# Kernel tuning notes

Hardware: AMD Instinct MI355X
Metric: run time of the kernel (lower is better)

Reference implementation:

```python
import jax, jax.numpy as jnp
import numpy as np

B, IN, H = 4096, 2048, 2048
STD = 1.0 / np.sqrt(H)


def setup_inputs() -> dict:
    key = jax.random.key(0)
    ks = jax.random.split(key, 16)
    uni = lambda k, shape: jax.random.uniform(k, shape, jnp.float32, -STD, STD)
    inp = {
        "x": jax.random.normal(ks[0], (B, IN), jnp.float32),
        "h": jax.random.normal(ks[1], (B, H), jnp.float32),
        "c": jax.random.normal(ks[2], (B, H), jnp.float32),
        # weights are used untransposed via th.mm(x, w): w_x* must be [IN, H]-compatible,
        # which in the original requires IN == H; shapes kept as [H, IN].
        "w_xi": uni(ks[3], (H, IN)), "w_xf": uni(ks[4], (H, IN)),
        "w_xo": uni(ks[5], (H, IN)), "w_xc": uni(ks[6], (H, IN)),
        "w_hi": uni(ks[7], (H, H)), "w_hf": uni(ks[8], (H, H)),
        "w_ho": uni(ks[9], (H, H)), "w_hc": uni(ks[10], (H, H)),
        "b_i": uni(ks[11], (H,)), "b_f": uni(ks[12], (H,)),
        "b_o": uni(ks[13], (H,)), "b_c": uni(ks[14], (H,)),
    }
    return inp


def reference(x, h, c, w_xi, w_xf, w_xo, w_xc, w_hi, w_hf, w_ho, w_hc,
              b_i, b_f, b_o, b_c):
    # Fused form of the 8 small GEMMs: concat gate weights along output dim.
    Wx = jnp.concatenate([w_xi, w_xf, w_xo, w_xc], axis=1)  # [IN, 4H]
    Wh = jnp.concatenate([w_hi, w_hf, w_ho, w_hc], axis=1)  # [H, 4H]
    b = jnp.concatenate([b_i, b_f, b_o, b_c])               # [4H]
    gates = x @ Wx + h @ Wh + b                              # [B, 4H]
    i_t, f_t, o_t, g_t = jnp.split(gates, 4, axis=1)
    i_t = jax.nn.sigmoid(i_t)
    f_t = jax.nn.sigmoid(f_t)
    o_t = jax.nn.sigmoid(o_t)
    g_t = jnp.tanh(g_t)
    c_t = c * f_t + i_t * g_t
    h_t = o_t * jnp.tanh(c_t)
    # original reshapes to [B, 1, H]
    return h_t[:, None, :], c_t[:, None, :]
```

## Files before the change

kernel.cpp:

```cpp
#include <hip/hip_runtime.h>
#include <stdint.h>

typedef unsigned short u16;
typedef __bf16 bf16x8 __attribute__((ext_vector_type(8)));
typedef float f32x4 __attribute__((ext_vector_type(4)));
typedef unsigned short u16x8 __attribute__((ext_vector_type(8)));
typedef unsigned short u16x4 __attribute__((ext_vector_type(4)));

#define B_ROWS 4096
#define H_DIM  2048
#define K_DIM  4096
#define N_DIM  8192

__device__ __forceinline__ u16 f2b(float f) {
  union { float f; unsigned int i; } v; v.f = f;
  unsigned int i = v.i;
  return (u16)((i + 0x7fffu + ((i >> 16) & 1u)) >> 16);
}
__device__ __forceinline__ float b2f(u16 u) {
  union { unsigned int i; float f; } v; v.i = ((unsigned int)u) << 16; return v.f;
}
__device__ __forceinline__ float sigmoidf_(float x) { return 1.0f / (1.0f + __expf(-x)); }
__device__ __forceinline__ float tanhf_(float x)    { return 1.0f - 2.0f / (__expf(2.0f * x) + 1.0f); }

__device__ __forceinline__ void glds16(const u16* g, u16* l) {
  __builtin_amdgcn_global_load_lds(
      (__attribute__((address_space(1))) void*)(g),
      (__attribute__((address_space(3))) void*)(l), 16, 0, 0);
}

__device__ __forceinline__ uint32_t lds_off(const void* p) {
  return (uint32_t)(uintptr_t)(__attribute__((address_space(3))) const void*)p;
}

__device__ __forceinline__ bf16x8 ds_read128(uint32_t byte_off) {
  bf16x8 r;
  asm volatile("ds_read_b128 %0, %1" : "=&v"(r) : "v"(byte_off));
  return r;
}
__device__ __forceinline__ bf16x8 ds_read128_hi(uint32_t byte_off) {
  bf16x8 r;
  asm volatile("ds_read_b128 %0, %1 offset:4096" : "=&v"(r) : "v"(byte_off));
  return r;
}
#define SCHED_FENCE __builtin_amdgcn_sched_barrier(0)

struct WPtrs { const float* p[8]; };

__global__ __launch_bounds__(256) void prep_all(WPtrs wp,
                                                const float* __restrict__ X,
                                                const float* __restrict__ Hs,
                                                u16* __restrict__ Wt,
                                                u16* __restrict__ Abf) {
  __shared__ float tile[64][65];
  const int z = blockIdx.z;
  const int tid = threadIdx.x;
  if (z < 8) {
    const int s = z >> 2, g = z & 3;
    const float* __restrict__ w = wp.p[z];
    const int j0 = blockIdx.x * 64, k0 = blockIdx.y * 64;

    const int c4 = (tid & 15) * 4;
    const int r0 = tid >> 4;
#pragma unroll
    for (int it = 0; it < 4; ++it) {
      int r = r0 + it * 16;
      float4 v = *(const float4*)(w + (size_t)(k0 + r) * H_DIM + j0 + c4);
      tile[r][c4 + 0] = v.x;
      tile[r][c4 + 1] = v.y;
      tile[r][c4 + 2] = v.z;
      tile[r][c4 + 3] = v.w;
    }
    __syncthreads();

    const int cc = (tid & 7) * 8;
    const int jr0 = tid >> 3;
#pragma unroll
    for (int it = 0; it < 2; ++it) {
      int jr = jr0 + it * 32;
      u16x8 v;
#pragma unroll
      for (int i = 0; i < 8; ++i) v[i] = f2b(tile[cc + i][jr]);
      size_t orow = (size_t)(g * H_DIM + j0 + jr);
      *(u16x8*)(Wt + orow * K_DIM + (size_t)(s * H_DIM + k0 + cc)) = v;
    }
  } else {
    const int cid = (z - 8) * 1024 + blockIdx.y * 32 + blockIdx.x;
#pragma unroll
    for (int t = 0; t < 4; ++t) {
      const size_t chunk = (size_t)cid * 1024 + t * 256 + tid;
      const int b = (int)(chunk >> 9);
      const int c = ((int)chunk & 511) * 8;
      const float* src = (c < H_DIM) ? (X + (size_t)b * H_DIM + c)
                                     : (Hs + (size_t)b * H_DIM + (c - H_DIM));
      float4 v0 = *(const float4*)(src);
      float4 v1 = *(const float4*)(src + 4);
      u16x8 o;
      o[0] = f2b(v0.x); o[1] = f2b(v0.y); o[2] = f2b(v0.z); o[3] = f2b(v0.w);
      o[4] = f2b(v1.x); o[5] = f2b(v1.y); o[6] = f2b(v1.z); o[7] = f2b(v1.w);
      *(u16x8*)(Abf + chunk * 8) = o;
    }
  }
}

__global__ __launch_bounds__(512, 2) void gemm_gates(const u16* __restrict__ A,
                                                     const u16* __restrict__ Wt,
                                                     u16* __restrict__ gates) {
  __shared__ __align__(16) u16 sA[4 * 256 * 32];
  __shared__ __align__(16) u16 sB[4 * 256 * 32];
  const int tid = threadIdx.x;
  const int wave = tid >> 6, lane = tid & 63;
  const int wm = wave >> 2, wn = wave & 3;

  const int wg = (blockIdx.x & 7) * 64 + (blockIdx.x >> 3);
  const int bm = wg & 15;
  const int bn = wg >> 4;

  const int c0 = wave * 2;
  const int rs0 = c0 * 16 + (lane >> 2);
  const int rs1 = rs0 + 16;
  const int kc0 = (lane & 3) ^ ((rs0 >> 1) & 3);
  const int kc1 = (lane & 3) ^ ((rs1 >> 1) & 3);
  const size_t gA0 = (size_t)(bm * 256 + rs0) * K_DIM + kc0 * 8;
  const size_t gA1 = (size_t)(bm * 256 + rs1) * K_DIM + kc1 * 8;
  const size_t gB0 = (size_t)(bn * 256 + rs0) * K_DIM + kc0 * 8;
  const size_t gB1 = (size_t)(bn * 256 + rs1) * K_DIM + kc1 * 8;

  const int q = lane >> 4;
  uint32_t aOffB[4], bOffB[4];
#pragma unroll
  for (int i = 0; i < 4; ++i) {
    int ra = wm * 128 + i * 16 + (lane & 15);
    aOffB[i] = (uint32_t)(ra * 32 + ((q ^ ((ra >> 1) & 3)) * 8)) * 2u;
  }
#pragma unroll
  for (int i = 0; i < 4; ++i) {
    int rb = wn * 64 + i * 16 + (lane & 15);
    bOffB[i] = (uint32_t)(rb * 32 + ((q ^ ((rb >> 1) & 3)) * 8)) * 2u;
  }
  const uint32_t sAb = lds_off(sA);
  const uint32_t sBb = lds_off(sB);

  f32x4 acc[8][4] = {};
  const int NT = K_DIM / 32;

  bf16x8 af[4], ag[4], bfE[4], bfO[4];

#pragma unroll
  for (int t = 0; t < 3; ++t) {
    const size_t ko = (size_t)t * 32;
    u16* da = sA + t * 8192;
    u16* db = sB + t * 8192;
    glds16(A  + gA0 + ko, da + c0 * 512);
    glds16(A  + gA1 + ko, da + (c0 + 1) * 512);
    glds16(Wt + gB0 + ko, db + c0 * 512);
    glds16(Wt + gB1 + ko, db + (c0 + 1) * 512);
  }
  asm volatile("s_waitcnt vmcnt(8)" ::: "memory");
  __builtin_amdgcn_s_barrier();
  SCHED_FENCE;
#pragma unroll
  for (int i = 0; i < 4; ++i) af[i]  = ds_read128(sAb + aOffB[i]);
#pragma unroll
  for (int i = 0; i < 4; ++i) bfE[i] = ds_read128(sBb + bOffB[i]);

#define TILE_BODY(T, BFC, BFN)                                                 \
  {                                                                            \
    const int pf = (T) + 3;                                                    \
    const uint32_t aSlot = sAb + (uint32_t)((T) & 3) * 16384u;                 \
    const bool dopf = pf < NT;                                                 \
    const size_t ko = (size_t)pf * 32;                                         \
    if (dopf) {                                                                \
      u16* dA = sA + (pf & 3) * 8192;                                          \
      glds16(A + gA0 + ko, dA + c0 * 512);                                     \
      glds16(A + gA1 + ko, dA + (c0 + 1) * 512);                               \
    }                                                                          \
                                       \
    _Pragma("unroll")                                                          \
    for (int i = 0; i < 4; ++i) ag[i] = ds_read128_hi(aSlot + aOffB[i]);       \
     \
    asm volatile("s_waitcnt lgkmcnt(4)" ::: "memory");                         \
    SCHED_FENCE;                                                               \
    __builtin_amdgcn_s_setprio(1);                                             \
    _Pragma("unroll")                                                          \
    for (int mi = 0; mi < 4; ++mi)                                             \
      _Pragma("unroll")                                                        \
      for (int ni = 0; ni < 4; ++ni)                                           \
        acc[mi][ni] = __builtin_amdgcn_mfma_f32_16x16x32_bf16(                 \
            af[mi], BFC[ni], acc[mi][ni], 0, 0, 0);                            \
    __builtin_amdgcn_s_setprio(0);                                             \
    if (dopf) {                                                                \
      u16* dB = sB + (pf & 3) * 8192;                                          \
      glds16(Wt + gB0 + ko, dB + c0 * 512);                                    \
      glds16(Wt + gB1 + ko, dB + (c0 + 1) * 512);                              \
    }                                                                          \
       \
    if ((T) < NT - 3)       { asm volatile("s_waitcnt vmcnt(8) lgkmcnt(0)" ::: "memory"); } \
    else if ((T) == NT - 3) { asm volatile("s_waitcnt vmcnt(4) lgkmcnt(0)" ::: "memory"); } \
    else if ((T) == NT - 2) { asm volatile("s_waitcnt vmcnt(0) lgkmcnt(0)" ::: "memory"); } \
    else                    { asm volatile("s_waitcnt lgkmcnt(0)" ::: "memory"); }          \
    if ((T) < NT - 1) __builtin_amdgcn_s_barrier();                            \
    SCHED_FENCE;                                                               \
                                  \
    if ((T) + 1 < NT) {                                                        \
      const uint32_t aN = sAb + (uint32_t)(((T) + 1) & 3) * 16384u;            \
      const uint32_t bN = sBb + (uint32_t)(((T) + 1) & 3) * 16384u;            \
      _Pragma("unroll")                                                        \
      for (int i = 0; i < 4; ++i) af[i]  = ds_read128(aN + aOffB[i]);          \
      _Pragma("unroll")                                                        \
      for (int i = 0; i < 4; ++i) BFN[i] = ds_read128(bN + bOffB[i]);          \
    }                                                                          \
                   \
    __builtin_amdgcn_s_setprio(1);                                             \
    _Pragma("unroll")                                                          \
    for (int mi = 0; mi < 4; ++mi)                                             \
      _Pragma("unroll")                                                        \
      for (int ni = 0; ni < 4; ++ni)                                           \
        acc[4 + mi][ni] = __builtin_amdgcn_mfma_f32_16x16x32_bf16(             \
            ag[mi], BFC[ni], acc[4 + mi][ni], 0, 0, 0);                        \
    __builtin_amdgcn_s_setprio(0);                                             \
  }

  for (int T2 = 0; T2 < NT; T2 += 2) {
    TILE_BODY(T2,     bfE, bfO);
    TILE_BODY(T2 + 1, bfO, bfE);
  }
#undef TILE_BODY

  const int rbase = bm * 256 + wm * 128 + (lane >> 4) * 4;
  const int cbase = bn * 256 + wn * 64 + (lane & 15);
#pragma unroll
  for (int mi = 0; mi < 8; ++mi) {
#pragma unroll
    for (int ni = 0; ni < 4; ++ni) {
      size_t base = (size_t)(rbase + mi * 16) * N_DIM + (size_t)(cbase + ni * 16);
#pragma unroll
      for (int r = 0; r < 4; ++r)
        gates[base + (size_t)r * N_DIM] = f2b(acc[mi][ni][r]);
    }
  }
}

__global__ __launch_bounds__(256) void lstm_epilogue(
    const u16* __restrict__ gates, const float* __restrict__ Cin,
    const float* __restrict__ Bi, const float* __restrict__ Bf,
    const float* __restrict__ Bo, const float* __restrict__ Bc,
    float* __restrict__ Out) {
  const int idx = blockIdx.x * 256 + threadIdx.x;
  const int b = idx >> 9;
  const int j = (idx & 511) * 4;
  const size_t gbase = (size_t)b * N_DIM + j;
  u16x4 iv = *(const u16x4*)(gates + gbase);
  u16x4 fv = *(const u16x4*)(gates + gbase + 2048);
  u16x4 ov = *(const u16x4*)(gates + gbase + 4096);
  u16x4 gv = *(const u16x4*)(gates + gbase + 6144);
  float4 cv  = *(const float4*)(Cin + (size_t)b * H_DIM + j);
  float4 biv = *(const float4*)(Bi + j);
  float4 bfv = *(const float4*)(Bf + j);
  float4 bov = *(const float4*)(Bo + j);
  float4 bcv = *(const float4*)(Bc + j);
  float ce[4] = {cv.x, cv.y, cv.z, cv.w};
  float bie[4] = {biv.x, biv.y, biv.z, biv.w};
  float bfe[4] = {bfv.x, bfv.y, bfv.z, bfv.w};
  float boe[4] = {bov.x, bov.y, bov.z, bov.w};
  float bce[4] = {bcv.x, bcv.y, bcv.z, bcv.w};
  float4 hv, ctv;
  float he[4], cte[4];
#pragma unroll
  for (int e = 0; e < 4; ++e) {
    float it = sigmoidf_(b2f(iv[e]) + bie[e]);
    float ft = sigmoidf_(b2f(fv[e]) + bfe[e]);
    float ot = sigmoidf_(b2f(ov[e]) + boe[e]);
    float gt = tanhf_(b2f(gv[e]) + bce[e]);
    float ct = ce[e] * ft + it * gt;
    he[e] = ot * tanhf_(ct);
    cte[e] = ct;
  }
  hv.x = he[0]; hv.y = he[1]; hv.z = he[2]; hv.w = he[3];
  ctv.x = cte[0]; ctv.y = cte[1]; ctv.z = cte[2]; ctv.w = cte[3];
  *(float4*)(Out + (size_t)b * H_DIM + j) = hv;
  *(float4*)(Out + (size_t)B_ROWS * H_DIM + (size_t)b * H_DIM + j) = ctv;
}

extern "C" void kernel_launch(void* const* d_in, const int* in_sizes, int n_in,
                              void* d_out, int out_size, void* d_ws, size_t ws_size,
                              hipStream_t stream) {
  const float* X   = (const float*)d_in[0];
  const float* Hs  = (const float*)d_in[1];
  const float* Cin = (const float*)d_in[2];
  WPtrs wp;
  for (int i = 0; i < 8; ++i) wp.p[i] = (const float*)d_in[3 + i];
  const float* Bi = (const float*)d_in[11];
  const float* Bf = (const float*)d_in[12];
  const float* Bo = (const float*)d_in[13];
  const float* Bc = (const float*)d_in[14];

  u16* Wt    = (u16*)d_ws;
  u16* Abf   = Wt + (size_t)N_DIM * K_DIM;
  u16* gates = Abf + (size_t)B_ROWS * K_DIM;
  float* Out = (float*)d_out;

  prep_all<<<dim3(32, 32, 10), 256, 0, stream>>>(wp, X, Hs, Wt, Abf);
  gemm_gates<<<16 * 32, 512, 0, stream>>>(Abf, Wt, gates);
  lstm_epilogue<<<(B_ROWS * H_DIM / 4) / 256, 256, 0, stream>>>(gates, Cin, Bi, Bf, Bo, Bc, Out);
}
```

Baseline: 506.7 us.

## Fuse LSTM epilogue into GEMM via gate-interleaved N tiles and LDS staging

Each GEMM block now takes 64 hidden columns from each of the four gates (i,f,o,g), so all gates for a hidden unit land in the same block. Accumulators are converted to bf16 and staged transposed in LDS, then the block applies the sigmoid/tanh cell update and writes h and c directly. This removes the bf16 gates round trip through global memory and the separate epilogue launch. In exchange, the LDS footprint grows (GLS padding) and the epilogue's Cin/Out accesses are scalar but still coalesced across j.

```diff
diff --git a/kernel.cpp b/kernel.cpp
--- a/kernel.cpp
+++ b/kernel.cpp
@@ -103,18 +103,23 @@
   }
 }
 
-__global__ __launch_bounds__(512, 2) void gemm_gates(const u16* __restrict__ A,
-                                                     const u16* __restrict__ Wt,
-                                                     u16* __restrict__ gates) {
-  __shared__ __align__(16) u16 sA[4 * 256 * 32];
-  __shared__ __align__(16) u16 sB[4 * 256 * 32];
+#define GLS 260
+__global__ __launch_bounds__(512, 2) void gemm_fused(
+    const u16* __restrict__ A, const u16* __restrict__ Wt,
+    const float* __restrict__ Cin,
+    const float* __restrict__ Bi, const float* __restrict__ Bff,
+    const float* __restrict__ Bo, const float* __restrict__ Bc,
+    float* __restrict__ Out) {
+  __shared__ __align__(16) u16 smem[4 * 64 * GLS];
+  u16* sA = smem;
+  u16* sB = smem + 4 * 8192;
   const int tid = threadIdx.x;
   const int wave = tid >> 6, lane = tid & 63;
   const int wm = wave >> 2, wn = wave & 3;
 
   const int wg = (blockIdx.x & 7) * 64 + (blockIdx.x >> 3);
   const int bm = wg & 15;
-  const int bn = wg >> 4;
+  const int bj = wg >> 4;
 
   const int c0 = wave * 2;
   const int rs0 = c0 * 16 + (lane >> 2);
@@ -123,8 +128,10 @@
   const int kc1 = (lane & 3) ^ ((rs1 >> 1) & 3);
   const size_t gA0 = (size_t)(bm * 256 + rs0) * K_DIM + kc0 * 8;
   const size_t gA1 = (size_t)(bm * 256 + rs1) * K_DIM + kc1 * 8;
-  const size_t gB0 = (size_t)(bn * 256 + rs0) * K_DIM + kc0 * 8;
-  const size_t gB1 = (size_t)(bn * 256 + rs1) * K_DIM + kc1 * 8;
+  const int nB0 = (rs0 >> 6) * 2048 + bj * 64 + (rs0 & 63);
+  const int nB1 = (rs1 >> 6) * 2048 + bj * 64 + (rs1 & 63);
+  const size_t gB0 = (size_t)nB0 * K_DIM + kc0 * 8;
+  const size_t gB1 = (size_t)nB1 * K_DIM + kc1 * 8;
 
   const int q = lane >> 4;
   uint32_t aOffB[4], bOffB[4];
@@ -227,59 +234,54 @@
   }
 #undef TILE_BODY
 
-  const int rbase = bm * 256 + wm * 128 + (lane >> 4) * 4;
-  const int cbase = bn * 256 + wn * 64 + (lane & 15);
-#pragma unroll
-  for (int mi = 0; mi < 8; ++mi) {
-#pragma unroll
-    for (int ni = 0; ni < 4; ++ni) {
-      size_t base = (size_t)(rbase + mi * 16) * N_DIM + (size_t)(cbase + ni * 16);
-#pragma unroll
-      for (int r = 0; r < 4; ++r)
-        gates[base + (size_t)r * N_DIM] = f2b(acc[mi][ni][r]);
-    }
-  }
-}
-
-__global__ __launch_bounds__(256) void lstm_epilogue(
-    const u16* __restrict__ gates, const float* __restrict__ Cin,
-    const float* __restrict__ Bi, const float* __restrict__ Bf,
-    const float* __restrict__ Bo, const float* __restrict__ Bc,
-    float* __restrict__ Out) {
-  const int idx = blockIdx.x * 256 + threadIdx.x;
-  const int b = idx >> 9;
-  const int j = (idx & 511) * 4;
-  const size_t gbase = (size_t)b * N_DIM + j;
-  u16x4 iv = *(const u16x4*)(gates + gbase);
-  u16x4 fv = *(const u16x4*)(gates + gbase + 2048);
-  u16x4 ov = *(const u16x4*)(gates + gbase + 4096);
-  u16x4 gv = *(const u16x4*)(gates + gbase + 6144);
-  float4 cv  = *(const float4*)(Cin + (size_t)b * H_DIM + j);
-  float4 biv = *(const float4*)(Bi + j);
-  float4 bfv = *(const float4*)(Bf + j);
-  float4 bov = *(const float4*)(Bo + j);
-  float4 bcv = *(const float4*)(Bc + j);
-  float ce[4] = {cv.x, cv.y, cv.z, cv.w};
-  float bie[4] = {biv.x, biv.y, biv.z, biv.w};
-  float bfe[4] = {bfv.x, bfv.y, bfv.z, bfv.w};
-  float boe[4] = {bov.x, bov.y, bov.z, bov.w};
-  float bce[4] = {bcv.x, bcv.y, bcv.z, bcv.w};
-  float4 hv, ctv;
-  float he[4], cte[4];
-#pragma unroll
-  for (int e = 0; e < 4; ++e) {
-    float it = sigmoidf_(b2f(iv[e]) + bie[e]);
-    float ft = sigmoidf_(b2f(fv[e]) + bfe[e]);
-    float ot = sigmoidf_(b2f(ov[e]) + boe[e]);
-    float gt = tanhf_(b2f(gv[e]) + bce[e]);
-    float ct = ce[e] * ft + it * gt;
-    he[e] = ot * tanhf_(ct);
-    cte[e] = ct;
-  }
-  hv.x = he[0]; hv.y = he[1]; hv.z = he[2]; hv.w = he[3];
-  ctv.x = cte[0]; ctv.y = cte[1]; ctv.z = cte[2]; ctv.w = cte[3];
-  *(float4*)(Out + (size_t)b * H_DIM + j) = hv;
-  *(float4*)(Out + (size_t)B_ROWS * H_DIM + (size_t)b * H_DIM + j) = ctv;
+  __syncthreads();
+  u16* gl = smem;
+  {
+    const int rowb = wm * 128 + (lane >> 4) * 4;
+    const int jb   = lane & 15;
+#pragma unroll
+    for (int mi = 0; mi < 8; ++mi) {
+#pragma unroll
+      for (int ni = 0; ni < 4; ++ni) {
+        const int row = rowb + mi * 16;
+        const int j = jb + ni * 16;
+        u16x4 o;
+#pragma unroll
+        for (int r = 0; r < 4; ++r) o[r] = f2b(acc[mi][ni][r]);
+        *(u16x4*)(gl + (size_t)(wn * 64 + j) * GLS + row) = o;
+      }
+    }
+  }
+  __syncthreads();
+
+  {
+    const int j = tid & 63;
+    const int rg = tid >> 6;
+    const int jg = bj * 64 + j;
+    const float bi = Bi[jg], bf_ = Bff[jg], bo = Bo[jg], bc = Bc[jg];
+    const size_t CH = (size_t)B_ROWS * H_DIM;
+#pragma unroll
+    for (int it = 0; it < 8; ++it) {
+      const int row = rg * 4 + it * 32;
+      u16x4 iv = *(const u16x4*)(gl + (size_t)(0 * 64 + j) * GLS + row);
+      u16x4 fv = *(const u16x4*)(gl + (size_t)(1 * 64 + j) * GLS + row);
+      u16x4 ov = *(const u16x4*)(gl + (size_t)(2 * 64 + j) * GLS + row);
+      u16x4 gv = *(const u16x4*)(gl + (size_t)(3 * 64 + j) * GLS + row);
+      const size_t grow = (size_t)(bm * 256 + row);
+#pragma unroll
+      for (int k = 0; k < 4; ++k) {
+        const size_t gidx = (grow + k) * H_DIM + jg;
+        float cold = Cin[gidx];
+        float it_ = sigmoidf_(b2f(iv[k]) + bi);
+        float ft_ = sigmoidf_(b2f(fv[k]) + bf_);
+        float ot_ = sigmoidf_(b2f(ov[k]) + bo);
+        float gt_ = tanhf_(b2f(gv[k]) + bc);
+        float ct  = cold * ft_ + it_ * gt_;
+        Out[gidx]      = ot_ * tanhf_(ct);
+        Out[CH + gidx] = ct;
+      }
+    }
+  }
 }
 
 extern "C" void kernel_launch(void* const* d_in, const int* in_sizes, int n_in,
@@ -297,10 +299,8 @@
 
   u16* Wt    = (u16*)d_ws;
   u16* Abf   = Wt + (size_t)N_DIM * K_DIM;
-  u16* gates = Abf + (size_t)B_ROWS * K_DIM;
   float* Out = (float*)d_out;
 
   prep_all<<<dim3(32, 32, 10), 256, 0, stream>>>(wp, X, Hs, Wt, Abf);
-  gemm_gates<<<16 * 32, 512, 0, stream>>>(Abf, Wt, gates);
-  lstm_epilogue<<<(B_ROWS * H_DIM / 4) / 256, 256, 0, stream>>>(gates, Cin, Bi, Bf, Bo, Bc, Out);
-}
+  gemm_fused<<<16 * 32, 512, 0, stream>>>(Abf, Wt, Cin, Bi, Bf, Bo, Bc, Out);
+}
```

Result: faster. 493.5 us (-2.6%).
